# Performance work log

Hardware: AMD Instinct MI355X
Metric: run time of the kernel (lower is better)

Reference implementation:

```python
import jax, jax.numpy as jnp
import numpy as np

B, S, HID = 1, 2048, 2048
NH, NKV = 16, 4
HD = HID // NH  # 128


def _rope_manual(x, cos_h, sin_h):
    # x: [B, S, nh, HD]; cos_h/sin_h: [1, S, 1, HD//2]
    d = x.shape[-1]
    x_rot = x[..., : d // 2]
    x_pass = x[..., d // 2:]
    # rotate interleaved pairs inside the first half
    x_rot = jnp.stack([-x_rot[..., 1::2], x_rot[..., ::2]], axis=-1)
    x_rot = x_rot.reshape(x_rot.shape[:-2] + (d // 2,))
    return jnp.concatenate(
        [x_rot * cos_h + x_pass * sin_h, -x_rot * sin_h + x_pass * cos_h], axis=-1
    )


def setup_inputs() -> dict:
    key = jax.random.key(0)
    ks = jax.random.split(key, 7)
    bound = 1.0 / np.sqrt(HID)
    return {
        "x": jax.random.normal(ks[0], (B, S, HID), jnp.float32),
        "cos": jax.random.uniform(ks[1], (S, HD), jnp.float32),
        "sin": jax.random.uniform(ks[2], (S, HD), jnp.float32),
        "wq": jax.random.uniform(ks[3], (NH * HD, HID), jnp.float32, -bound, bound),
        "wk": jax.random.uniform(ks[4], (NKV * HD, HID), jnp.float32, -bound, bound),
        "wv": jax.random.uniform(ks[5], (NKV * HD, HID), jnp.float32, -bound, bound),
        "wo": jax.random.uniform(ks[6], (HID, HID), jnp.float32, -bound, bound),
    }


def reference(x, cos, sin, wq, wk, wv, wo):
    b, s, _ = x.shape
    q = jnp.einsum("bsh,oh->bso", x, wq).reshape(b, s, NH, HD)
    k = jnp.einsum("bsh,oh->bso", x, wk).reshape(b, s, NKV, HD)
    v = jnp.einsum("bsh,oh->bso", x, wv).reshape(b, s, NKV, HD)

    cos_h = cos[None, :, None, : HD // 2]  # [1,S,1,HD/2]
    sin_h = sin[None, :, None, : HD // 2]
    q = _rope_manual(q, cos_h, sin_h)
    k = _rope_manual(k, cos_h, sin_h)

    # [B, H, S, D]
    q = q.transpose(0, 2, 1, 3)
    k = k.transpose(0, 2, 1, 3)
    v = v.transpose(0, 2, 1, 3)
    # GQA kv repeat (repeat_interleave over head dim)
    rep = NH // NKV
    k = jnp.repeat(k, rep, axis=1)
    v = jnp.repeat(v, rep, axis=1)

    scale = 1.0 / np.sqrt(HD).astype(np.float32)
    scores = jnp.einsum("bhqd,bhkd->bhqk", q, k) * scale
    causal = jnp.tril(jnp.ones((s, s), bool))
    scores = jnp.where(causal[None, None], scores, jnp.finfo(scores.dtype).min)
    attn = jax.nn.softmax(scores, axis=-1)
    out = jnp.einsum("bhqk,bhkd->bhqd", attn, v)  # [B,H,S,D]
    out = out.transpose(0, 2, 1, 3).reshape(b, s, NH * HD)
    return jnp.einsum("bso,ho->bsh", out, wo)
```

## Files before the change

kernel.cpp:

```cpp
#include <hip/hip_runtime.h>
#include <hip/hip_bf16.h>

typedef __bf16 bf16_t;
typedef __attribute__((ext_vector_type(8))) __bf16 bf16x8;
typedef __attribute__((ext_vector_type(4))) __bf16 bf16x4;
typedef __attribute__((ext_vector_type(4))) float f32x4;

#define S_LEN 2048
#define HID 2048
#define NH 16
#define NKV 4
#define HD 128

__device__ __forceinline__ void gll16(const bf16_t* g, bf16_t* l) {
    __builtin_amdgcn_global_load_lds(
        (const __attribute__((address_space(1))) unsigned int*)g,
        (__attribute__((address_space(3))) unsigned int*)l, 16, 0, 0);
}

__device__ __forceinline__ bf16x8 cvt2x4(float4 a, float4 b) {
    bf16x8 o;
    o[0]=(bf16_t)a.x; o[1]=(bf16_t)a.y; o[2]=(bf16_t)a.z; o[3]=(bf16_t)a.w;
    o[4]=(bf16_t)b.x; o[5]=(bf16_t)b.y; o[6]=(bf16_t)b.z; o[7]=(bf16_t)b.w;
    return o;
}

__global__ __launch_bounds__(256) void cvt_all(
    const float* __restrict__ x,  const float* __restrict__ wq,
    const float* __restrict__ wk, const float* __restrict__ wv,
    const float* __restrict__ wo, bf16_t* __restrict__ xb,
    bf16_t* __restrict__ wb, bf16_t* __restrict__ wob)
{
    const size_t M = 1024 * 1024;
    size_t g = ((size_t)blockIdx.x * 256 + threadIdx.x) * 8;
    const float* src; bf16_t* dst; size_t soff, doff;
    if (g < 4 * M) {
        src = x; dst = xb; soff = g; doff = g;
    } else if (g < 10 * M) {
        size_t w = g - 4 * M; dst = wb; doff = w;
        if (w < 4 * M)      { src = wq; soff = w; }
        else if (w < 5 * M) { src = wk; soff = w - 4 * M; }
        else                { src = wv; soff = w - 5 * M; }
    } else {
        src = wo; dst = wob; soff = g - 10 * M; doff = soff;
    }
    float4 a = *(const float4*)&src[soff];
    float4 b = *(const float4*)&src[soff + 4];
    *(bf16x8*)&dst[doff] = cvt2x4(a, b);
}

template<int MODE, typename CT>
__global__ __launch_bounds__(256, 4) void gemm128x64(
    const bf16_t* __restrict__ A, const bf16_t* __restrict__ B,
    CT* __restrict__ C, bf16_t* __restrict__ CkP, bf16_t* __restrict__ CvtP,
    int N, int K)
{
    __shared__ __align__(16) bf16_t sA[2][128 * 64];
    __shared__ __align__(16) bf16_t sB[2][64 * 64];

    const int tid = threadIdx.x, lane = tid & 63, wave = tid >> 6;
    const int l16 = lane & 15, quad = lane >> 4;
    const int m0 = blockIdx.y * 128, n0 = blockIdx.x * 64;
    const int wm = (wave >> 1) * 64, wn = (wave & 1) * 32;

    const bf16_t* gA[4]; const bf16_t* gB[2];
    int laOff[4], lbOff[2];
#pragma unroll
    for (int t = 0; t < 4; t++) {
        int p = (wave * 4 + t) * 64 + lane;
        int row = p >> 3;
        int lc = (p & 7) ^ (row & 7);
        gA[t] = A + (size_t)(m0 + row) * K + lc * 8;
        laOff[t] = (wave * 4 + t) * 512;
    }
#pragma unroll
    for (int t = 0; t < 2; t++) {
        int p = (wave * 2 + t) * 64 + lane;
        int row = p >> 3;
        int lc = (p & 7) ^ (row & 7);
        gB[t] = B + (size_t)(n0 + row) * K + lc * 8;
        lbOff[t] = (wave * 2 + t) * 512;
    }

    int offA[2][4], offB[2][2];
#pragma unroll
    for (int kc = 0; kc < 2; kc++) {
#pragma unroll
        for (int i = 0; i < 4; i++) {
            int rm = wm + i * 16 + l16;
            offA[kc][i] = rm * 64 + (((kc * 4 + quad) ^ (rm & 7)) * 8);
        }
#pragma unroll
        for (int j = 0; j < 2; j++) {
            int rn = wn + j * 16 + l16;
            offB[kc][j] = rn * 64 + (((kc * 4 + quad) ^ (rn & 7)) * 8);
        }
    }

    f32x4 acc[4][2] = {};

#pragma unroll
    for (int t = 0; t < 4; t++) { gll16(gA[t], &sA[0][laOff[t]]); gA[t] += 64; }
#pragma unroll
    for (int t = 0; t < 2; t++) { gll16(gB[t], &sB[0][lbOff[t]]); gB[t] += 64; }
    __syncthreads();

    int bsel = 0;
    for (int k0 = 0; k0 < K; k0 += 64) {
        const int ns = bsel ^ 1;
        if (k0 + 64 < K) {
#pragma unroll
            for (int t = 0; t < 4; t++) { gll16(gA[t], &sA[ns][laOff[t]]); gA[t] += 64; }
#pragma unroll
            for (int t = 0; t < 2; t++) { gll16(gB[t], &sB[ns][lbOff[t]]); gB[t] += 64; }
        }

#pragma unroll
        for (int kc = 0; kc < 2; kc++) {
            bf16x8 af[4], bfv[2];
#pragma unroll
            for (int i = 0; i < 4; i++) af[i] = *(bf16x8*)&sA[bsel][offA[kc][i]];
#pragma unroll
            for (int j = 0; j < 2; j++) bfv[j] = *(bf16x8*)&sB[bsel][offB[kc][j]];
#pragma unroll
            for (int i = 0; i < 4; i++)
#pragma unroll
                for (int j = 0; j < 2; j++)
                    acc[i][j] = __builtin_amdgcn_mfma_f32_16x16x32_bf16(af[i], bfv[j], acc[i][j], 0, 0, 0);
        }

        __syncthreads();
        bsel = ns;
    }

#pragma unroll
    for (int i = 0; i < 4; i++) {
        int rowb = m0 + wm + i * 16 + quad * 4;
#pragma unroll
        for (int j = 0; j < 2; j++) {
            int col = n0 + wn + j * 16 + l16;
#pragma unroll
            for (int r = 0; r < 4; r++) {
                float v = acc[i][j][r];
                int row = rowb + r;
                if (MODE == 0) {
                    C[(size_t)row * N + col] = (CT)v;
                } else {
                    if (col < 2048)      C[(size_t)row * 2048 + col] = (CT)v;
                    else if (col < 2560) CkP[(size_t)row * 512 + (col - 2048)] = (bf16_t)v;
                    else                 CvtP[(size_t)(col - 2560) * S_LEN + row] = (bf16_t)v;
                }
            }
        }
    }
}

__global__ void rope_all(bf16_t* __restrict__ Qh, bf16_t* __restrict__ Kh,
                         const float* __restrict__ cosb, const float* __restrict__ sinb)
{
    int s = blockIdx.x;
    int grp = blockIdx.y;
    int sub = threadIdx.x >> 5;
    int i = threadIdx.x & 31;
    bf16_t* row = (grp < 4) ? (Qh + ((size_t)s * NH + grp * 4 + sub) * HD)
                            : (Kh + ((size_t)s * NKV + sub) * HD);
    float x0 = (float)row[2 * i];
    float x1 = (float)row[2 * i + 1];
    float p0 = (float)row[64 + 2 * i];
    float p1 = (float)row[64 + 2 * i + 1];
    float c0 = cosb[s * HD + 2 * i];
    float c1 = cosb[s * HD + 2 * i + 1];
    float n0 = sinb[s * HD + 2 * i];
    float n1 = sinb[s * HD + 2 * i + 1];
    float r0 = -x1, r1 = x0;
    row[2 * i]          = (bf16_t)(r0 * c0 + p0 * n0);
    row[2 * i + 1]      = (bf16_t)(r1 * c1 + p1 * n1);
    row[64 + 2 * i]     = (bf16_t)(-r0 * n0 + p0 * c0);
    row[64 + 2 * i + 1] = (bf16_t)(-r1 * n1 + p1 * c1);
}

__global__ __launch_bounds__(256, 1) void flash_attn11(
    const bf16_t* __restrict__ Q,
    const bf16_t* __restrict__ Kb,
    const bf16_t* __restrict__ VT,
    bf16_t* __restrict__ OpD,
    bf16_t* __restrict__ OpX,
    float* __restrict__ lpart,
    int S)
{
    __shared__ __align__(16) bf16_t sK[2][64 * 136];
    __shared__ __align__(16) bf16_t sVT[2][128 * 72];
    __shared__ __align__(16) bf16_t sP[4][16 * 72];

    const int c   = blockIdx.x;
    const int kvh = blockIdx.y;
    const int p   = c >> 2, sub = c & 3;
    const int ts   = (33 * sub + 3) >> 2;
    const int tend = (33 * sub + 36) >> 2;
    const int tA   = p + 1;

    const int tid = threadIdx.x, lane = tid & 63, wave = tid >> 6;
    const int l16 = lane & 15, quad = lane >> 4;
    const int rowg = wave;
    const int h0   = kvh * 4;
    const float scale = 0.08838834764831845f;

    int krow[4], kcol[4], vrow[4], vcol[4];
#pragma unroll
    for (int it = 0; it < 4; it++) {
        int cc = tid + 256 * it;
        krow[it] = cc >> 4; kcol[it] = (cc & 15) * 8;
        vrow[it] = cc >> 3; vcol[it] = (cc & 7) * 8;
    }

#pragma unroll
    for (int sI = 0; sI < 2; sI++) {
        int st0, st1, sqt, ssl;
        if (sI == 0) {
            if (ts < tA) { st0 = ts; st1 = (tend < tA ? tend : tA); sqt = p;      ssl = c; }
            else         { st0 = ts; st1 = tend;                    sqt = 31 - p; ssl = c; }
        } else {
            if (!(ts < tA && tend > tA)) break;
            st0 = tA; st1 = tend; sqt = 31 - p; ssl = 64 + p;
        }
        const int base = (sqt == p) ? 0 : tA;
        const int kb = st0 - base, ke = st1 - base;
        const int qt = sqt;
        const int q0 = qt * 64;
        const int qrow = q0 + rowg * 16 + l16;

        bf16x8 qf[4][4];
#pragma unroll
        for (int h = 0; h < 4; h++)
#pragma unroll
            for (int cc = 0; cc < 4; cc++)
                qf[h][cc] = *(const bf16x8*)&Q[(size_t)qrow * HID + (h0 + h) * HD + cc * 32 + quad * 8];

        f32x4 oacc[4][8] = {};
        float lsum[4] = {0.f, 0.f, 0.f, 0.f};

        bf16x8 kpre[4], vpre[4];
#pragma unroll
        for (int it = 0; it < 4; it++) {
            kpre[it] = *(const bf16x8*)&Kb[(size_t)(kb * 64 + krow[it]) * (NKV * HD) + kvh * HD + kcol[it]];
            vpre[it] = *(const bf16x8*)&VT[((size_t)kvh * HD + vrow[it]) * S + kb * 64 + vcol[it]];
        }
#pragma unroll
        for (int it = 0; it < 4; it++) {
            *(bf16x8*)&sK[0][krow[it] * 136 + kcol[it]] = kpre[it];
            *(bf16x8*)&sVT[0][vrow[it] * 72 + vcol[it]] = vpre[it];
        }
        if (kb + 1 < ke) {
            const int t1 = (kb + 1) * 64;
#pragma unroll
            for (int it = 0; it < 4; it++) {
                kpre[it] = *(const bf16x8*)&Kb[(size_t)(t1 + krow[it]) * (NKV * HD) + kvh * HD + kcol[it]];
                vpre[it] = *(const bf16x8*)&VT[((size_t)kvh * HD + vrow[it]) * S + t1 + vcol[it]];
            }
        }
        __syncthreads();

        int sel = 0;
        for (int kt = kb; kt < ke; kt++) {
            const int t0 = kt * 64;
            const int ns = sel ^ 1;

            if (kt + 1 < ke) {
#pragma unroll
                for (int it = 0; it < 4; it++) {
                    *(bf16x8*)&sK[ns][krow[it] * 136 + kcol[it]] = kpre[it];
                    *(bf16x8*)&sVT[ns][vrow[it] * 72 + vcol[it]] = vpre[it];
                }
                if (kt + 2 < ke) {
                    const int t2 = t0 + 128;
#pragma unroll
                    for (int it = 0; it < 4; it++) {
                        kpre[it] = *(const bf16x8*)&Kb[(size_t)(t2 + krow[it]) * (NKV * HD) + kvh * HD + kcol[it]];
                        vpre[it] = *(const bf16x8*)&VT[((size_t)kvh * HD + vrow[it]) * S + t2 + vcol[it]];
                    }
                }
            }

            f32x4 sc[4][4];
            __builtin_amdgcn_s_setprio(1);
#pragma unroll
            for (int nt = 0; nt < 4; nt++) {
                bf16x8 kf[4];
#pragma unroll
                for (int cc = 0; cc < 4; cc++)
                    kf[cc] = *(bf16x8*)&sK[sel][(nt * 16 + l16) * 136 + cc * 32 + quad * 8];
#pragma unroll
                for (int h = 0; h < 4; h++) {
                    f32x4 d = {};
#pragma unroll
                    for (int cc = 0; cc < 4; cc++)
                        d = __builtin_amdgcn_mfma_f32_16x16x32_bf16(kf[cc], qf[h][cc], d, 0, 0, 0);
                    sc[h][nt] = d;
                }
            }
            __builtin_amdgcn_s_setprio(0);

            bf16x8 pa[4][2];
            if (kt == qt) {
#pragma unroll
                for (int h = 0; h < 4; h++) {
#pragma unroll
                    for (int nt = 0; nt < 4; nt++) {
                        const int tbk = t0 + nt * 16 + quad * 4;
                        bf16x4 pk;
#pragma unroll
                        for (int r = 0; r < 4; r++) {
                            float pv = (tbk + r <= qrow) ? __expf(sc[h][nt][r] * scale) : 0.0f;
                            lsum[h] += pv;
                            pk[r] = (bf16_t)pv;
                        }
                        *(bf16x4*)&sP[wave][l16 * 72 + nt * 16 + quad * 4] = pk;
                    }
#pragma unroll
                    for (int kc = 0; kc < 2; kc++)
                        pa[h][kc] = *(bf16x8*)&sP[wave][l16 * 72 + kc * 32 + quad * 8];
                }
            } else {
#pragma unroll
                for (int h = 0; h < 4; h++) {
#pragma unroll
                    for (int nt = 0; nt < 4; nt++) {
                        bf16x4 pk;
#pragma unroll
                        for (int r = 0; r < 4; r++) {
                            float pv = __expf(sc[h][nt][r] * scale);
                            lsum[h] += pv;
                            pk[r] = (bf16_t)pv;
                        }
                        *(bf16x4*)&sP[wave][l16 * 72 + nt * 16 + quad * 4] = pk;
                    }
#pragma unroll
                    for (int kc = 0; kc < 2; kc++)
                        pa[h][kc] = *(bf16x8*)&sP[wave][l16 * 72 + kc * 32 + quad * 8];
                }
            }

            __builtin_amdgcn_s_setprio(1);
#pragma unroll
            for (int dt = 0; dt < 8; dt++)
#pragma unroll
                for (int kc = 0; kc < 2; kc++) {
                    bf16x8 vf = *(bf16x8*)&sVT[sel][(dt * 16 + l16) * 72 + kc * 32 + quad * 8];
#pragma unroll
                    for (int h = 0; h < 4; h++)
                        oacc[h][dt] = __builtin_amdgcn_mfma_f32_16x16x32_bf16(pa[h][kc], vf, oacc[h][dt], 0, 0, 0);
                }
            __builtin_amdgcn_s_setprio(0);

            __syncthreads();
            sel = ns;
        }

        const int sg = kvh * 80 + ssl;
        bf16_t* Op = (sg < 256) ? (OpD + (size_t)sg * 32768)
                                : (OpX + (size_t)(sg - 256) * 32768);
#pragma unroll
        for (int h = 0; h < 4; h++) {
            float lr = lsum[h];
            lr += __shfl_xor(lr, 16, 64);
            lr += __shfl_xor(lr, 32, 64);
            if (quad == 0)
                lpart[(size_t)sg * 256 + (rowg * 16 + l16) * 4 + h] = lr;
#pragma unroll
            for (int r = 0; r < 4; r++) {
                int rr = rowg * 16 + quad * 4 + r;
#pragma unroll
                for (int dt = 0; dt < 8; dt++)
                    Op[((size_t)rr * 4 + h) * 128 + dt * 16 + l16] =
                        (bf16_t)(oacc[h][dt][r]);
            }
        }
    }
}

__global__ __launch_bounds__(256) void flash_combine10(
    const bf16_t* __restrict__ OpD, const bf16_t* __restrict__ OpX,
    const float* __restrict__ lpart, bf16_t* __restrict__ oh)
{
    int i = (blockIdx.x * 256 + threadIdx.x) * 8;
    int s = i >> 11;
    int h = (i >> 7) & 15;
    int col = i & 127;
    int qt = s >> 6;
    int base80 = (h >> 2) * 80;
    int roff = (s & 63) * 4 + (h & 3);

    int sl[4]; int nsl = 0;
    if (qt <= 15) {
        int pr = qt;
#pragma unroll
        for (int sub = 0; sub < 4; sub++) {
            int tss = (33 * sub + 3) >> 2;
            if (tss < qt + 1) sl[nsl++] = pr * 4 + sub;
        }
    } else {
        int pr = 31 - qt, tAh = pr + 1;
#pragma unroll
        for (int sub = 0; sub < 4; sub++) {
            int tss = (33 * sub + 3) >> 2;
            int ten = (33 * sub + 36) >> 2;
            if (ten > tAh) sl[nsl++] = (tss < tAh) ? 64 + pr : pr * 4 + sub;
        }
    }

    float acc[8] = {0.f, 0.f, 0.f, 0.f, 0.f, 0.f, 0.f, 0.f};
    float l = 0.f;
    for (int ci = 0; ci < nsl; ci++) {
        int sg = base80 + sl[ci];
        const bf16_t* P = (sg < 256) ? (OpD + (size_t)sg * 32768)
                                     : (OpX + (size_t)(sg - 256) * 32768);
        bf16x8 a = *(const bf16x8*)&P[(size_t)roff * 128 + col];
#pragma unroll
        for (int j = 0; j < 8; j++) acc[j] += (float)a[j];
        l += lpart[(size_t)sg * 256 + roff];
    }
    float inv = 1.0f / l;
    bf16x8 o;
#pragma unroll
    for (int j = 0; j < 8; j++)
        o[j] = (bf16_t)(acc[j] * inv);
    *(bf16x8*)&oh[i] = o;
}

extern "C" void kernel_launch(void* const* d_in, const int* in_sizes, int n_in,
                              void* d_out, int out_size, void* d_ws, size_t ws_size,
                              hipStream_t stream)
{
    const float* x    = (const float*)d_in[0];
    const float* cosb = (const float*)d_in[1];
    const float* sinb = (const float*)d_in[2];
    const float* wq   = (const float*)d_in[3];
    const float* wk   = (const float*)d_in[4];
    const float* wv   = (const float*)d_in[5];
    const float* wo   = (const float*)d_in[6];
    float* out = (float*)d_out;

    char* ws = (char*)d_ws;
    bf16_t* wb = (bf16_t*)(ws);
    bf16_t* qh = (bf16_t*)(ws + (size_t)12 * 1024 * 1024);
    bf16_t* kh = (bf16_t*)(ws + (size_t)20 * 1024 * 1024);
    bf16_t* vT = (bf16_t*)(ws + (size_t)22 * 1024 * 1024);
    float*  lp = (float*) (ws + (size_t)24 * 1024 * 1024);
    bf16_t* opx = (bf16_t*)(ws + (size_t)24 * 1024 * 1024 + 512 * 1024);
    bf16_t* wob = (bf16_t*)(ws + (size_t)28 * 1024 * 1024 + 512 * 1024);
    bf16_t* xb  = (bf16_t*)d_out;
    bf16_t* opd = (bf16_t*)d_out;

    const int NX = S_LEN * HID;

    cvt_all<<<14 * 1024 * 1024 / (256 * 8), 256, 0, stream>>>(
        x, wq, wk, wv, wo, xb, wb, wob);

    gemm128x64<1, bf16_t><<<dim3(48, 16), 256, 0, stream>>>(xb, wb, qh, kh, vT, 3072, HID);

    rope_all<<<dim3(S_LEN, 5), 128, 0, stream>>>(qh, kh, cosb, sinb);

    flash_attn11<<<dim3(64, NKV), 256, 0, stream>>>(qh, kh, vT, opd, opx, lp, S_LEN);

    flash_combine10<<<NX / (256 * 8), 256, 0, stream>>>(opd, opx, lp, qh);

    gemm128x64<0, float><<<dim3(32, 16), 256, 0, stream>>>(qh, wob, out, nullptr, nullptr, HID, HID);
}
```

Measured before the change: 212.9 us.

## Fuse Q RoPE into flash attention Q-fragment load and batch P LDS reads

Applies rotary embedding to Q directly on the register fragments after they are loaded inside the attention kernel, so the standalone rope pass now only touches K. This removes a global read-modify-write of the whole Q tensor. The P staging buffer in shared memory is expanded per head, so all four heads' probabilities are written before any are read back, which reduces interleaved LDS write/read dependencies. The cost is more shared memory and extra per-block cos/sin loads and ALU work in the attention prologue.

Result: no change. 212.5 us, median of 2 (-0.2%).

```diff
diff --git a/kernel.cpp b/kernel.cpp
--- a/kernel.cpp
+++ b/kernel.cpp
@@ -155,15 +155,13 @@
     }
 }
 
-__global__ void rope_all(bf16_t* __restrict__ Qh, bf16_t* __restrict__ Kh,
-                         const float* __restrict__ cosb, const float* __restrict__ sinb)
+__global__ void rope_k(bf16_t* __restrict__ Kh,
+                       const float* __restrict__ cosb, const float* __restrict__ sinb)
 {
     int s = blockIdx.x;
-    int grp = blockIdx.y;
     int sub = threadIdx.x >> 5;
     int i = threadIdx.x & 31;
-    bf16_t* row = (grp < 4) ? (Qh + ((size_t)s * NH + grp * 4 + sub) * HD)
-                            : (Kh + ((size_t)s * NKV + sub) * HD);
+    bf16_t* row = Kh + ((size_t)s * NKV + sub) * HD;
     float x0 = (float)row[2 * i];
     float x1 = (float)row[2 * i + 1];
     float p0 = (float)row[64 + 2 * i];
@@ -179,10 +177,11 @@
     row[64 + 2 * i + 1] = (bf16_t)(-r1 * n1 + p1 * c1);
 }
 
-__global__ __launch_bounds__(256, 1) void flash_attn11(
+__global__ __launch_bounds__(256, 1) void flash_attn12(
     const bf16_t* __restrict__ Q,
     const bf16_t* __restrict__ Kb,
     const bf16_t* __restrict__ VT,
+    const float* __restrict__ cosb, const float* __restrict__ sinb,
     bf16_t* __restrict__ OpD,
     bf16_t* __restrict__ OpX,
     float* __restrict__ lpart,
@@ -190,7 +189,7 @@
 {
     __shared__ __align__(16) bf16_t sK[2][64 * 136];
     __shared__ __align__(16) bf16_t sVT[2][128 * 72];
-    __shared__ __align__(16) bf16_t sP[4][16 * 72];
+    __shared__ __align__(16) bf16_t sP[4][4][16 * 72];
 
     const int c   = blockIdx.x;
     const int kvh = blockIdx.y;
@@ -236,6 +235,40 @@
             for (int cc = 0; cc < 4; cc++)
                 qf[h][cc] = *(const bf16x8*)&Q[(size_t)qrow * HID + (h0 + h) * HD + cc * 32 + quad * 8];
 
+        {
+            float cs0[8], sn0[8], cs1[8], sn1[8];
+            const float* cb = cosb + (size_t)qrow * HD;
+            const float* sb = sinb + (size_t)qrow * HD;
+#pragma unroll
+            for (int e = 0; e < 8; e++) {
+                cs0[e] = cb[quad * 8 + e];      sn0[e] = sb[quad * 8 + e];
+                cs1[e] = cb[32 + quad * 8 + e]; sn1[e] = sb[32 + quad * 8 + e];
+            }
+#pragma unroll
+            for (int h = 0; h < 4; h++) {
+                bf16x8 lo0 = qf[h][0], hi0 = qf[h][2];
+                bf16x8 lo1 = qf[h][1], hi1 = qf[h][3];
+                bf16x8 a0, b0, a1, b1;
+#pragma unroll
+                for (int e = 0; e < 8; e += 2) {
+                    float x0 = (float)lo0[e], x1 = (float)lo0[e + 1];
+                    float p0 = (float)hi0[e], p1 = (float)hi0[e + 1];
+                    a0[e]     = (bf16_t)(-x1 * cs0[e]     + p0 * sn0[e]);
+                    a0[e + 1] = (bf16_t)( x0 * cs0[e + 1] + p1 * sn0[e + 1]);
+                    b0[e]     = (bf16_t)( x1 * sn0[e]     + p0 * cs0[e]);
+                    b0[e + 1] = (bf16_t)(-x0 * sn0[e + 1] + p1 * cs0[e + 1]);
+                    float y0 = (float)lo1[e], y1 = (float)lo1[e + 1];
+                    float q0v = (float)hi1[e], q1v = (float)hi1[e + 1];
+                    a1[e]     = (bf16_t)(-y1 * cs1[e]     + q0v * sn1[e]);
+                    a1[e + 1] = (bf16_t)( y0 * cs1[e + 1] + q1v * sn1[e + 1]);
+                    b1[e]     = (bf16_t)( y1 * sn1[e]     + q0v * cs1[e]);
+                    b1[e + 1] = (bf16_t)(-y0 * sn1[e + 1] + q1v * cs1[e + 1]);
+                }
+                qf[h][0] = a0; qf[h][2] = b0;
+                qf[h][1] = a1; qf[h][3] = b1;
+            }
+        }
+
         f32x4 oacc[4][8] = {};
         float lsum[4] = {0.f, 0.f, 0.f, 0.f};
 
@@ -300,10 +333,9 @@
             }
             __builtin_amdgcn_s_setprio(0);
 
-            bf16x8 pa[4][2];
             if (kt == qt) {
 #pragma unroll
-                for (int h = 0; h < 4; h++) {
+                for (int h = 0; h < 4; h++)
 #pragma unroll
                     for (int nt = 0; nt < 4; nt++) {
                         const int tbk = t0 + nt * 16 + quad * 4;
@@ -314,15 +346,11 @@
                             lsum[h] += pv;
                             pk[r] = (bf16_t)pv;
                         }
-                        *(bf16x4*)&sP[wave][l16 * 72 + nt * 16 + quad * 4] = pk;
+                        *(bf16x4*)&sP[wave][h][l16 * 72 + nt * 16 + quad * 4] = pk;
                     }
-#pragma unroll
-                    for (int kc = 0; kc < 2; kc++)
-                        pa[h][kc] = *(bf16x8*)&sP[wave][l16 * 72 + kc * 32 + quad * 8];
-                }
             } else {
 #pragma unroll
-                for (int h = 0; h < 4; h++) {
+                for (int h = 0; h < 4; h++)
 #pragma unroll
                     for (int nt = 0; nt < 4; nt++) {
                         bf16x4 pk;
@@ -332,13 +360,15 @@
                             lsum[h] += pv;
                             pk[r] = (bf16_t)pv;
                         }
-                        *(bf16x4*)&sP[wave][l16 * 72 + nt * 16 + quad * 4] = pk;
+                        *(bf16x4*)&sP[wave][h][l16 * 72 + nt * 16 + quad * 4] = pk;
                     }
-#pragma unroll
-                    for (int kc = 0; kc < 2; kc++)
-                        pa[h][kc] = *(bf16x8*)&sP[wave][l16 * 72 + kc * 32 + quad * 8];
-                }
-            }
+            }
+            bf16x8 pa[4][2];
+#pragma unroll
+            for (int h = 0; h < 4; h++)
+#pragma unroll
+                for (int kc = 0; kc < 2; kc++)
+                    pa[h][kc] = *(bf16x8*)&sP[wave][h][l16 * 72 + kc * 32 + quad * 8];
 
             __builtin_amdgcn_s_setprio(1);
 #pragma unroll
@@ -458,9 +488,10 @@
 
     gemm128x64<1, bf16_t><<<dim3(48, 16), 256, 0, stream>>>(xb, wb, qh, kh, vT, 3072, HID);
 
-    rope_all<<<dim3(S_LEN, 5), 128, 0, stream>>>(qh, kh, cosb, sinb);
-
-    flash_attn11<<<dim3(64, NKV), 256, 0, stream>>>(qh, kh, vT, opd, opx, lp, S_LEN);
+    rope_k<<<dim3(S_LEN, 1), 128, 0, stream>>>(kh, cosb, sinb);
+
+    flash_attn12<<<dim3(64, NKV), 256, 0, stream>>>(qh, kh, vT, cosb, sinb,
+                                                    opd, opx, lp, S_LEN);
 
     flash_combine10<<<NX / (256 * 8), 256, 0, stream>>>(opd, opx, lp, qh);
 
```
